# Kernel tuning notes

Hardware: AMD Instinct MI355X
Metric: run time of the kernel (lower is better)

Reference implementation:

```python
import jax, jax.numpy as jnp
import numpy as np

HIDDEN = 4096
NUM_EXPERTS = 64
TOP_K = 2
N_TOKENS = 16384


def setup_inputs() -> dict:
    key = jax.random.key(0)
    kx, kw = jax.random.split(key)
    x = jax.random.normal(kx, (N_TOKENS, HIDDEN), dtype=jnp.float32)
    # nn.Linear(hidden, num_experts, bias=False) weight: [num_experts, hidden]
    gate_w = jax.random.normal(kw, (NUM_EXPERTS, HIDDEN), dtype=jnp.float32) * (HIDDEN ** -0.5)
    return {"x": x, "gate_w": gate_w}


def reference(x, gate_w):
    # logits: [N, num_experts]
    logits = jnp.einsum("nh,eh->ne", x, gate_w)
    topk_vals, topk_idx = jax.lax.top_k(logits, TOP_K)  # [N, k]
    topk_gates = jax.nn.softmax(topk_vals, axis=-1)
    return topk_gates, topk_idx
```

## Files before the change

kernel.cpp:

```cpp
#include <hip/hip_runtime.h>

#define NTOK 16384
#define HID  4096
#define NEXP 64
#define BM   32
#define BK   64
#define NSTEPS (HID / BK)
#define PLANE  (NEXP * HID)

typedef _Float16 f16;
typedef f16  f16x4 __attribute__((ext_vector_type(4)));
typedef f16  f16x8 __attribute__((ext_vector_type(8)));
typedef float f32x4 __attribute__((ext_vector_type(4)));

__device__ __forceinline__ int swz(int row, int unit16) {
    return row * 64 + ((unit16 ^ (row & 7)) << 3);
}

__global__ __launch_bounds__(256)
void pack_w_kernel(const float* __restrict__ w, f16* __restrict__ wp) {
    int tid = blockIdx.x * 256 + threadIdx.x;
    int e = tid >> 9;
    int k = (tid & 511) << 3;
    const float* src = w + (size_t)e * HID + k;
    float4 v0 = *(const float4*)(src);
    float4 v1 = *(const float4*)(src + 4);
    float sv[8] = {v0.x, v0.y, v0.z, v0.w, v1.x, v1.y, v1.z, v1.w};
    f16x8 hi, lo;
    #pragma unroll
    for (int j = 0; j < 8; ++j) {
        float s = sv[j] * 64.0f;
        f16 h = (f16)s;
        hi[j] = h;
        lo[j] = (f16)(s - (float)h);
    }
    int ks   = k >> 5;
    int g    = e >> 4;
    int lane = ((k >> 3) & 3) * 16 + (e & 15);
    size_t dst = ((size_t)(ks * 4 + g) * 64 + lane) * 8;
    *(f16x8*)&wp[dst]         = hi;
    *(f16x8*)&wp[PLANE + dst] = lo;
}

__global__ __launch_bounds__(512, 4)
void topk_gate_kernel(const float* __restrict__ x,
                      const f16* __restrict__ wp,
                      float* __restrict__ out) {
    __shared__ __align__(16) f16 Ah[2][BM * BK];
    __shared__ __align__(16) f16 Al[2][BM * BK];
    __shared__ float red[4][BM][4];

    const int t    = threadIdx.x;
    const int blk  = blockIdx.x;
    const int lane = t & 63;
    const int wid  = t >> 6;
    const int wm   = wid & 1;
    const int wn   = wid >> 1;
    const int col  = lane & 15;
    const int grp  = lane >> 4;

    const int srow = t >> 4;
    const int sq4  = t & 15;
    const float* asrc = x + ((size_t)blk * BM + srow) * HID + sq4 * 4;
    const int aoff = swz(srow, sq4 >> 1) + (sq4 & 1) * 4;

    const f16* bp = wp + ((size_t)(wn * 64 + lane)) * 8;

    f32x4 acc = {0.f, 0.f, 0.f, 0.f};
    const int arow = wm * 16 + col;

    float4 a_cur = *(const float4*)(asrc);
    {
        float4 v = a_cur;
        f16 hx=(f16)v.x, hy=(f16)v.y, hz=(f16)v.z, hw=(f16)v.w;
        *(f16x4*)&Ah[0][aoff] = (f16x4){hx,hy,hz,hw};
        *(f16x4*)&Al[0][aoff] = (f16x4){(f16)(v.x-(float)hx),(f16)(v.y-(float)hy),
                                        (f16)(v.z-(float)hz),(f16)(v.w-(float)hw)};
    }
    float4 a_nxt = *(const float4*)(asrc + BK);
    f16x8 bh0c = *(const f16x8*)(bp + 0);
    f16x8 bl0c = *(const f16x8*)(bp + PLANE + 0);
    f16x8 bh1c = *(const f16x8*)(bp + 2048);
    f16x8 bl1c = *(const f16x8*)(bp + PLANE + 2048);
    __syncthreads();

    for (int s = 0; s < NSTEPS; ++s) {
        const int buf = s & 1;
        const int sn = (s + 1 < NSTEPS) ? (s + 1) : s;
        const size_t bo = (size_t)sn * 4096;
        f16x8 bh0n = *(const f16x8*)(bp + bo);
        f16x8 bl0n = *(const f16x8*)(bp + PLANE + bo);
        f16x8 bh1n = *(const f16x8*)(bp + bo + 2048);
        f16x8 bl1n = *(const f16x8*)(bp + PLANE + bo + 2048);
        float4 a_n2 = (s + 2 < NSTEPS) ? *(const float4*)(asrc + (size_t)(s + 2) * BK)
                                       : a_nxt;

        {
            f16x8 ah = *(const f16x8*)&Ah[buf][swz(arow, grp)];
            f16x8 al = *(const f16x8*)&Al[buf][swz(arow, grp)];
            acc = __builtin_amdgcn_mfma_f32_16x16x32_f16(ah, bh0c, acc, 0, 0, 0);
            acc = __builtin_amdgcn_mfma_f32_16x16x32_f16(ah, bl0c, acc, 0, 0, 0);
            acc = __builtin_amdgcn_mfma_f32_16x16x32_f16(al, bh0c, acc, 0, 0, 0);
            ah = *(const f16x8*)&Ah[buf][swz(arow, 4 + grp)];
            al = *(const f16x8*)&Al[buf][swz(arow, 4 + grp)];
            acc = __builtin_amdgcn_mfma_f32_16x16x32_f16(ah, bh1c, acc, 0, 0, 0);
            acc = __builtin_amdgcn_mfma_f32_16x16x32_f16(ah, bl1c, acc, 0, 0, 0);
            acc = __builtin_amdgcn_mfma_f32_16x16x32_f16(al, bh1c, acc, 0, 0, 0);
        }

        if (s + 1 < NSTEPS) {
            float4 v = a_nxt;
            f16 hx=(f16)v.x, hy=(f16)v.y, hz=(f16)v.z, hw=(f16)v.w;
            *(f16x4*)&Ah[buf ^ 1][aoff] = (f16x4){hx,hy,hz,hw};
            *(f16x4*)&Al[buf ^ 1][aoff] = (f16x4){(f16)(v.x-(float)hx),(f16)(v.y-(float)hy),
                                                  (f16)(v.z-(float)hz),(f16)(v.w-(float)hw)};
        }
        __syncthreads();

        a_nxt = a_n2;
        bh0c = bh0n; bl0c = bl0n; bh1c = bh1n; bl1c = bl1n;
    }

    #pragma unroll
    for (int r = 0; r < 4; ++r) {
        float v0 = acc[r]; int i0 = wn * 16 + col;
        float v1 = -INFINITY; int i1 = 0x7fffffff;
        #pragma unroll
        for (int m = 1; m <= 8; m <<= 1) {
            float ov0 = __shfl_xor(v0, m, 64);
            int   oi0 = __shfl_xor(i0, m, 64);
            float ov1 = __shfl_xor(v1, m, 64);
            int   oi1 = __shfl_xor(i1, m, 64);
            bool ob = (ov0 > v0) || (ov0 == v0 && oi0 < i0);
            if (ob) {
                bool k2 = (v0 > ov1) || (v0 == ov1 && i0 < oi1);
                v1 = k2 ? v0 : ov1; i1 = k2 ? i0 : oi1;
                v0 = ov0; i0 = oi0;
            } else {
                bool k2 = (ov0 > v1) || (ov0 == v1 && oi0 < i1);
                v1 = k2 ? ov0 : v1; i1 = k2 ? oi0 : i1;
            }
        }
        if (col == 0) {
            int tl = wm * 16 + grp * 4 + r;
            red[wn][tl][0] = v0; red[wn][tl][1] = (float)i0;
            red[wn][tl][2] = v1; red[wn][tl][3] = (float)i1;
        }
    }
    __syncthreads();

    if (t < BM) {
        float v0 = red[0][t][0]; int i0 = (int)red[0][t][1];
        float v1 = red[0][t][2]; int i1 = (int)red[0][t][3];
        #pragma unroll
        for (int g = 1; g < 4; ++g) {
            float b0 = red[g][t][0]; int bi0 = (int)red[g][t][1];
            float b1 = red[g][t][2]; int bi1 = (int)red[g][t][3];
            bool bb = (b0 > v0) || (b0 == v0 && bi0 < i0);
            if (bb) {
                bool k2 = (v0 > b1) || (v0 == b1 && i0 < bi1);
                float nv1 = k2 ? v0 : b1; int ni1 = k2 ? i0 : bi1;
                v0 = b0; i0 = bi0; v1 = nv1; i1 = ni1;
            } else {
                bool k2 = (b0 > v1) || (b0 == v1 && bi0 < i1);
                v1 = k2 ? b0 : v1; i1 = k2 ? bi0 : i1;
            }
        }
        float d  = (v1 - v0) * (1.0f / 64.0f);
        float e  = expf(d);
        float g0 = 1.0f / (1.0f + e);
        float g1 = e / (1.0f + e);

        int tok = blk * BM + t;
        out[(size_t)tok * 2 + 0] = g0;
        out[(size_t)tok * 2 + 1] = g1;
        out[(size_t)NTOK * 2 + (size_t)tok * 2 + 0] = (float)i0;
        out[(size_t)NTOK * 2 + (size_t)tok * 2 + 1] = (float)i1;
    }
}

extern "C" void kernel_launch(void* const* d_in, const int* in_sizes, int n_in,
                              void* d_out, int out_size, void* d_ws, size_t ws_size,
                              hipStream_t stream) {
    const float* x = (const float*)d_in[0];
    const float* w = (const float*)d_in[1];
    float* out = (float*)d_out;
    f16* wp = (f16*)d_ws;
    (void)in_sizes; (void)n_in; (void)out_size; (void)ws_size;

    pack_w_kernel<<<dim3(128), dim3(256), 0, stream>>>(w, wp);
    topk_gate_kernel<<<dim3(NTOK / BM), dim3(512), 0, stream>>>(x, wp, out);
}
```

Before: 78.78 us.

## Split K across waves with register-direct A loads and LDS partial-sum reduction

Restructures the gate GEMM so each of four waves covers a quarter of the hidden dimension for all 32 tokens and all 64 experts. A is loaded straight from global memory into registers and split into f16 hi/lo there, which removes the shared-memory staging and the per-step barriers. Partial logits are then summed through LDS, and each wave runs a 64-lane top-2 shuffle reduction per token. This raises per-wave MFMA work and register pressure, and the direct A loads read 32 bytes per row per lane, so coalescing may be worse than before.

New measurement: 73.13 us. 7.2% less time.

```diff
diff --git a/kernel.cpp b/kernel.cpp
--- a/kernel.cpp
+++ b/kernel.cpp
@@ -3,19 +3,15 @@
 #define NTOK 16384
 #define HID  4096
 #define NEXP 64
-#define BM   32
-#define BK   64
-#define NSTEPS (HID / BK)
+#define TOKB 32
+#define KSPLIT 4
+#define STEPS (HID / KSPLIT / 64)
 #define PLANE  (NEXP * HID)
+#define LROW 68
 
 typedef _Float16 f16;
-typedef f16  f16x4 __attribute__((ext_vector_type(4)));
 typedef f16  f16x8 __attribute__((ext_vector_type(8)));
 typedef float f32x4 __attribute__((ext_vector_type(4)));
-
-__device__ __forceinline__ int swz(int row, int unit16) {
-    return row * 64 + ((unit16 ^ (row & 7)) << 3);
-}
 
 __global__ __launch_bounds__(256)
 void pack_w_kernel(const float* __restrict__ w, f16* __restrict__ wp) {
@@ -42,91 +38,129 @@
     *(f16x8*)&wp[PLANE + dst] = lo;
 }
 
-__global__ __launch_bounds__(512, 4)
+__device__ __forceinline__ void cvt_hilo(float4 a, float4 b, f16x8& hi, f16x8& lo) {
+    float v[8] = {a.x, a.y, a.z, a.w, b.x, b.y, b.z, b.w};
+    #pragma unroll
+    for (int j = 0; j < 8; ++j) {
+        f16 h = (f16)v[j];
+        hi[j] = h;
+        lo[j] = (f16)(v[j] - (float)h);
+    }
+}
+
+__global__ __launch_bounds__(256)
 void topk_gate_kernel(const float* __restrict__ x,
                       const f16* __restrict__ wp,
                       float* __restrict__ out) {
-    __shared__ __align__(16) f16 Ah[2][BM * BK];
-    __shared__ __align__(16) f16 Al[2][BM * BK];
-    __shared__ float red[4][BM][4];
+    __shared__ float P[KSPLIT][TOKB * LROW];
+    __shared__ float F[TOKB * LROW];
 
     const int t    = threadIdx.x;
     const int blk  = blockIdx.x;
     const int lane = t & 63;
-    const int wid  = t >> 6;
-    const int wm   = wid & 1;
-    const int wn   = wid >> 1;
+    const int w    = t >> 6;
     const int col  = lane & 15;
     const int grp  = lane >> 4;
 
-    const int srow = t >> 4;
-    const int sq4  = t & 15;
-    const float* asrc = x + ((size_t)blk * BM + srow) * HID + sq4 * 4;
-    const int aoff = swz(srow, sq4 >> 1) + (sq4 & 1) * 4;
-
-    const f16* bp = wp + ((size_t)(wn * 64 + lane)) * 8;
-
-    f32x4 acc = {0.f, 0.f, 0.f, 0.f};
-    const int arow = wm * 16 + col;
-
-    float4 a_cur = *(const float4*)(asrc);
+    const float* aw = x + ((size_t)blk * TOKB + col) * HID + w * (HID / KSPLIT) + grp * 8;
+    const f16* bw = wp + (size_t)lane * 8;
+
+    f32x4 acc[2][4];
+    #pragma unroll
+    for (int tm = 0; tm < 2; ++tm)
+        #pragma unroll
+        for (int eg = 0; eg < 4; ++eg)
+            acc[tm][eg] = (f32x4){0.f, 0.f, 0.f, 0.f};
+
+    float4 af[2][2][2];
+    #pragma unroll
+    for (int tm = 0; tm < 2; ++tm)
+        #pragma unroll
+        for (int ks = 0; ks < 2; ++ks)
+            #pragma unroll
+            for (int h = 0; h < 2; ++h)
+                af[tm][ks][h] = *(const float4*)(aw + tm * 16 * HID + ks * 32 + h * 4);
+
+    for (int s = 0; s < STEPS; ++s) {
+        f16x8 bh[2][4], bl[2][4];
+        #pragma unroll
+        for (int ks = 0; ks < 2; ++ks) {
+            const size_t base = (size_t)((w * 32 + s * 2 + ks) * 4) * 512;
+            #pragma unroll
+            for (int eg = 0; eg < 4; ++eg) {
+                bh[ks][eg] = *(const f16x8*)(bw + base + eg * 512);
+                bl[ks][eg] = *(const f16x8*)(bw + base + eg * 512 + PLANE);
+            }
+        }
+        const int sn = (s + 1 < STEPS) ? (s + 1) : s;
+        float4 an[2][2][2];
+        #pragma unroll
+        for (int tm = 0; tm < 2; ++tm)
+            #pragma unroll
+            for (int ks = 0; ks < 2; ++ks)
+                #pragma unroll
+                for (int h = 0; h < 2; ++h)
+                    an[tm][ks][h] = *(const float4*)(aw + tm * 16 * HID + sn * 64 + ks * 32 + h * 4);
+
+        f16x8 ah[2][2], al[2][2];
+        #pragma unroll
+        for (int tm = 0; tm < 2; ++tm)
+            #pragma unroll
+            for (int ks = 0; ks < 2; ++ks)
+                cvt_hilo(af[tm][ks][0], af[tm][ks][1], ah[tm][ks], al[tm][ks]);
+
+        #pragma unroll
+        for (int ks = 0; ks < 2; ++ks)
+            #pragma unroll
+            for (int tm = 0; tm < 2; ++tm)
+                #pragma unroll
+                for (int eg = 0; eg < 4; ++eg) {
+                    acc[tm][eg] = __builtin_amdgcn_mfma_f32_16x16x32_f16(ah[tm][ks], bh[ks][eg], acc[tm][eg], 0, 0, 0);
+                    acc[tm][eg] = __builtin_amdgcn_mfma_f32_16x16x32_f16(ah[tm][ks], bl[ks][eg], acc[tm][eg], 0, 0, 0);
+                    acc[tm][eg] = __builtin_amdgcn_mfma_f32_16x16x32_f16(al[tm][ks], bh[ks][eg], acc[tm][eg], 0, 0, 0);
+                }
+
+        #pragma unroll
+        for (int tm = 0; tm < 2; ++tm)
+            #pragma unroll
+            for (int ks = 0; ks < 2; ++ks)
+                #pragma unroll
+                for (int h = 0; h < 2; ++h)
+                    af[tm][ks][h] = an[tm][ks][h];
+    }
+
+    #pragma unroll
+    for (int tm = 0; tm < 2; ++tm)
+        #pragma unroll
+        for (int eg = 0; eg < 4; ++eg)
+            #pragma unroll
+            for (int r = 0; r < 4; ++r) {
+                int tokl = tm * 16 + grp * 4 + r;
+                int e    = eg * 16 + col;
+                P[w][tokl * LROW + e] = acc[tm][eg][r];
+            }
+    __syncthreads();
+
     {
-        float4 v = a_cur;
-        f16 hx=(f16)v.x, hy=(f16)v.y, hz=(f16)v.z, hw=(f16)v.w;
-        *(f16x4*)&Ah[0][aoff] = (f16x4){hx,hy,hz,hw};
-        *(f16x4*)&Al[0][aoff] = (f16x4){(f16)(v.x-(float)hx),(f16)(v.y-(float)hy),
-                                        (f16)(v.z-(float)hz),(f16)(v.w-(float)hw)};
-    }
-    float4 a_nxt = *(const float4*)(asrc + BK);
-    f16x8 bh0c = *(const f16x8*)(bp + 0);
-    f16x8 bl0c = *(const f16x8*)(bp + PLANE + 0);
-    f16x8 bh1c = *(const f16x8*)(bp + 2048);
-    f16x8 bl1c = *(const f16x8*)(bp + PLANE + 2048);
+        int tok = t >> 3;
+        int e0  = (t & 7) * 8;
+        #pragma unroll
+        for (int j = 0; j < 8; ++j) {
+            float ssum = P[0][tok * LROW + e0 + j];
+            #pragma unroll
+            for (int w2 = 1; w2 < KSPLIT; ++w2)
+                ssum += P[w2][tok * LROW + e0 + j];
+            F[tok * LROW + e0 + j] = ssum;
+        }
+    }
     __syncthreads();
 
-    for (int s = 0; s < NSTEPS; ++s) {
-        const int buf = s & 1;
-        const int sn = (s + 1 < NSTEPS) ? (s + 1) : s;
-        const size_t bo = (size_t)sn * 4096;
-        f16x8 bh0n = *(const f16x8*)(bp + bo);
-        f16x8 bl0n = *(const f16x8*)(bp + PLANE + bo);
-        f16x8 bh1n = *(const f16x8*)(bp + bo + 2048);
-        f16x8 bl1n = *(const f16x8*)(bp + PLANE + bo + 2048);
-        float4 a_n2 = (s + 2 < NSTEPS) ? *(const float4*)(asrc + (size_t)(s + 2) * BK)
-                                       : a_nxt;
-
-        {
-            f16x8 ah = *(const f16x8*)&Ah[buf][swz(arow, grp)];
-            f16x8 al = *(const f16x8*)&Al[buf][swz(arow, grp)];
-            acc = __builtin_amdgcn_mfma_f32_16x16x32_f16(ah, bh0c, acc, 0, 0, 0);
-            acc = __builtin_amdgcn_mfma_f32_16x16x32_f16(ah, bl0c, acc, 0, 0, 0);
-            acc = __builtin_amdgcn_mfma_f32_16x16x32_f16(al, bh0c, acc, 0, 0, 0);
-            ah = *(const f16x8*)&Ah[buf][swz(arow, 4 + grp)];
-            al = *(const f16x8*)&Al[buf][swz(arow, 4 + grp)];
-            acc = __builtin_amdgcn_mfma_f32_16x16x32_f16(ah, bh1c, acc, 0, 0, 0);
-            acc = __builtin_amdgcn_mfma_f32_16x16x32_f16(ah, bl1c, acc, 0, 0, 0);
-            acc = __builtin_amdgcn_mfma_f32_16x16x32_f16(al, bh1c, acc, 0, 0, 0);
-        }
-
-        if (s + 1 < NSTEPS) {
-            float4 v = a_nxt;
-            f16 hx=(f16)v.x, hy=(f16)v.y, hz=(f16)v.z, hw=(f16)v.w;
-            *(f16x4*)&Ah[buf ^ 1][aoff] = (f16x4){hx,hy,hz,hw};
-            *(f16x4*)&Al[buf ^ 1][aoff] = (f16x4){(f16)(v.x-(float)hx),(f16)(v.y-(float)hy),
-                                                  (f16)(v.z-(float)hz),(f16)(v.w-(float)hw)};
-        }
-        __syncthreads();
-
-        a_nxt = a_n2;
-        bh0c = bh0n; bl0c = bl0n; bh1c = bh1n; bl1c = bl1n;
-    }
-
-    #pragma unroll
-    for (int r = 0; r < 4; ++r) {
-        float v0 = acc[r]; int i0 = wn * 16 + col;
-        float v1 = -INFINITY; int i1 = 0x7fffffff;
-        #pragma unroll
-        for (int m = 1; m <= 8; m <<= 1) {
+    for (int tt = 0; tt < 8; ++tt) {
+        int tokl = w * 8 + tt;
+        float v0 = F[tokl * LROW + lane]; int i0 = lane;
+        float v1 = -INFINITY;             int i1 = 0x7fffffff;
+        #pragma unroll
+        for (int m = 1; m <= 32; m <<= 1) {
             float ov0 = __shfl_xor(v0, m, 64);
             int   oi0 = __shfl_xor(i0, m, 64);
             float ov1 = __shfl_xor(v1, m, 64);
@@ -141,41 +175,17 @@
                 v1 = k2 ? ov0 : v1; i1 = k2 ? oi0 : i1;
             }
         }
-        if (col == 0) {
-            int tl = wm * 16 + grp * 4 + r;
-            red[wn][tl][0] = v0; red[wn][tl][1] = (float)i0;
-            red[wn][tl][2] = v1; red[wn][tl][3] = (float)i1;
-        }
-    }
-    __syncthreads();
-
-    if (t < BM) {
-        float v0 = red[0][t][0]; int i0 = (int)red[0][t][1];
-        float v1 = red[0][t][2]; int i1 = (int)red[0][t][3];
-        #pragma unroll
-        for (int g = 1; g < 4; ++g) {
-            float b0 = red[g][t][0]; int bi0 = (int)red[g][t][1];
-            float b1 = red[g][t][2]; int bi1 = (int)red[g][t][3];
-            bool bb = (b0 > v0) || (b0 == v0 && bi0 < i0);
-            if (bb) {
-                bool k2 = (v0 > b1) || (v0 == b1 && i0 < bi1);
-                float nv1 = k2 ? v0 : b1; int ni1 = k2 ? i0 : bi1;
-                v0 = b0; i0 = bi0; v1 = nv1; i1 = ni1;
-            } else {
-                bool k2 = (b0 > v1) || (b0 == v1 && bi0 < i1);
-                v1 = k2 ? b0 : v1; i1 = k2 ? bi0 : i1;
-            }
-        }
-        float d  = (v1 - v0) * (1.0f / 64.0f);
-        float e  = expf(d);
-        float g0 = 1.0f / (1.0f + e);
-        float g1 = e / (1.0f + e);
-
-        int tok = blk * BM + t;
-        out[(size_t)tok * 2 + 0] = g0;
-        out[(size_t)tok * 2 + 1] = g1;
-        out[(size_t)NTOK * 2 + (size_t)tok * 2 + 0] = (float)i0;
-        out[(size_t)NTOK * 2 + (size_t)tok * 2 + 1] = (float)i1;
+        if (lane == 0) {
+            float d  = (v1 - v0) * (1.0f / 64.0f);
+            float e  = expf(d);
+            float g0 = 1.0f / (1.0f + e);
+            float g1 = e / (1.0f + e);
+            int tok = blk * TOKB + tokl;
+            out[(size_t)tok * 2 + 0] = g0;
+            out[(size_t)tok * 2 + 1] = g1;
+            out[(size_t)NTOK * 2 + (size_t)tok * 2 + 0] = (float)i0;
+            out[(size_t)NTOK * 2 + (size_t)tok * 2 + 1] = (float)i1;
+        }
     }
 }
 
@@ -189,5 +199,5 @@
     (void)in_sizes; (void)n_in; (void)out_size; (void)ws_size;
 
     pack_w_kernel<<<dim3(128), dim3(256), 0, stream>>>(w, wp);
-    topk_gate_kernel<<<dim3(NTOK / BM), dim3(512), 0, stream>>>(x, wp, out);
-}
+    topk_gate_kernel<<<dim3(NTOK / TOKB), dim3(256), 0, stream>>>(x, wp, out);
+}
```

## Stream activations via direct global-to-LDS loads with triple-buffered pipeline

Applied to the files above, without the earlier changes.

Replaces the register-staged fp32 load and split-to-fp16 store with global_load_lds DMA straight into a three-deep LDS ring of raw fp32 activations. The hi/lo fp16 split now happens after reading from LDS, right before the MFMAs. Weight fragments are prefetched two steps ahead, and a manual vmcnt wait plus one barrier per step replaces the old end-of-step sync. This is meant to hide global latency and cut VGPR staging traffic, but it doubles the LDS footprint per buffer and relies on a hand-tuned vmcnt count being correct.

Measured after the change: 96.64 us. 22.7% more time.

```diff
diff --git a/kernel.cpp b/kernel.cpp
--- a/kernel.cpp
+++ b/kernel.cpp
@@ -1,21 +1,19 @@
 #include <hip/hip_runtime.h>
+#include <stdint.h>
 
 #define NTOK 16384
 #define HID  4096
 #define NEXP 64
-#define BM   32
-#define BK   64
-#define NSTEPS (HID / BK)
-#define PLANE  (NEXP * HID)
+#define TOKB 32
+#define NSTEPS 64
+#define PLANE (NEXP * HID)
 
 typedef _Float16 f16;
-typedef f16  f16x4 __attribute__((ext_vector_type(4)));
 typedef f16  f16x8 __attribute__((ext_vector_type(8)));
 typedef float f32x4 __attribute__((ext_vector_type(4)));
 
-__device__ __forceinline__ int swz(int row, int unit16) {
-    return row * 64 + ((unit16 ^ (row & 7)) << 3);
-}
+typedef __attribute__((address_space(3))) uint32_t  lds_u32;
+typedef __attribute__((address_space(1))) const uint32_t glb_u32;
 
 __global__ __launch_bounds__(256)
 void pack_w_kernel(const float* __restrict__ w, f16* __restrict__ wp) {
@@ -46,84 +44,100 @@
 void topk_gate_kernel(const float* __restrict__ x,
                       const f16* __restrict__ wp,
                       float* __restrict__ out) {
-    __shared__ __align__(16) f16 Ah[2][BM * BK];
-    __shared__ __align__(16) f16 Al[2][BM * BK];
-    __shared__ float red[4][BM][4];
+    __shared__ __align__(16) float Abuf[3][TOKB * 64];
+    __shared__ float red[4][TOKB][4];
 
     const int t    = threadIdx.x;
     const int blk  = blockIdx.x;
     const int lane = t & 63;
-    const int wid  = t >> 6;
-    const int wm   = wid & 1;
-    const int wn   = wid >> 1;
+    const int w    = t >> 6;
+    const int tm   = w & 1;
+    const int eg   = w >> 1;
     const int col  = lane & 15;
     const int grp  = lane >> 4;
 
-    const int srow = t >> 4;
-    const int sq4  = t & 15;
-    const float* asrc = x + ((size_t)blk * BM + srow) * HID + sq4 * 4;
-    const int aoff = swz(srow, sq4 >> 1) + (sq4 & 1) * 4;
-
-    const f16* bp = wp + ((size_t)(wn * 64 + lane)) * 8;
+    const int srow  = 4 * w + grp;
+    const int sunit = col ^ (srow & 7);
+    const float* asrc = x + ((size_t)blk * TOKB + srow) * HID + sunit * 4;
+
+    int fragOff[2][2];
+    {
+        const int arow = tm * 16 + col;
+        #pragma unroll
+        for (int ks = 0; ks < 2; ++ks)
+            #pragma unroll
+            for (int h = 0; h < 2; ++h)
+                fragOff[ks][h] = arow * 256 + ((ks * 8 + grp * 2 + h) ^ (arow & 7)) * 16;
+    }
+
+    const f16* bw = wp + ((size_t)eg * 64 + lane) * 8;
 
     f32x4 acc = {0.f, 0.f, 0.f, 0.f};
-    const int arow = wm * 16 + col;
-
-    float4 a_cur = *(const float4*)(asrc);
-    {
-        float4 v = a_cur;
-        f16 hx=(f16)v.x, hy=(f16)v.y, hz=(f16)v.z, hw=(f16)v.w;
-        *(f16x4*)&Ah[0][aoff] = (f16x4){hx,hy,hz,hw};
-        *(f16x4*)&Al[0][aoff] = (f16x4){(f16)(v.x-(float)hx),(f16)(v.y-(float)hy),
-                                        (f16)(v.z-(float)hz),(f16)(v.w-(float)hw)};
-    }
-    float4 a_nxt = *(const float4*)(asrc + BK);
-    f16x8 bh0c = *(const f16x8*)(bp + 0);
-    f16x8 bl0c = *(const f16x8*)(bp + PLANE + 0);
-    f16x8 bh1c = *(const f16x8*)(bp + 2048);
-    f16x8 bl1c = *(const f16x8*)(bp + PLANE + 2048);
-    __syncthreads();
-
+
+    #define STAGE(s_, b_) do {                                                    \
+        __builtin_amdgcn_global_load_lds(                                         \
+            (glb_u32*)(const void*)(asrc + (size_t)(s_) * 64),                    \
+            (lds_u32*)(void*)(&Abuf[b_][w * 256]), 16, 0, 0);                     \
+    } while (0)
+
+    f16x8 bh0[2], bl0[2], bh1[2], bl1[2], bh2[2], bl2[2];
+    #define BLOAD(s_, BH, BL) do {                                                \
+        _Pragma("unroll")                                                         \
+        for (int ks = 0; ks < 2; ++ks) {                                          \
+            size_t off_ = (size_t)(2 * (s_) + ks) * 2048;                         \
+            BH[ks] = *(const f16x8*)(bw + off_);                                  \
+            BL[ks] = *(const f16x8*)(bw + off_ + PLANE);                          \
+        }                                                                         \
+    } while (0)
+
+    STAGE(0, 0);
+    BLOAD(0, bh0, bl0);
+    asm volatile("" ::: "memory");
+    BLOAD(1, bh1, bl1);
+    asm volatile("" ::: "memory");
+    STAGE(1, 1);
+
+    int bufc = 0;
     for (int s = 0; s < NSTEPS; ++s) {
-        const int buf = s & 1;
-        const int sn = (s + 1 < NSTEPS) ? (s + 1) : s;
-        const size_t bo = (size_t)sn * 4096;
-        f16x8 bh0n = *(const f16x8*)(bp + bo);
-        f16x8 bl0n = *(const f16x8*)(bp + PLANE + bo);
-        f16x8 bh1n = *(const f16x8*)(bp + bo + 2048);
-        f16x8 bl1n = *(const f16x8*)(bp + PLANE + bo + 2048);
-        float4 a_n2 = (s + 2 < NSTEPS) ? *(const float4*)(asrc + (size_t)(s + 2) * BK)
-                                       : a_nxt;
-
-        {
-            f16x8 ah = *(const f16x8*)&Ah[buf][swz(arow, grp)];
-            f16x8 al = *(const f16x8*)&Al[buf][swz(arow, grp)];
-            acc = __builtin_amdgcn_mfma_f32_16x16x32_f16(ah, bh0c, acc, 0, 0, 0);
-            acc = __builtin_amdgcn_mfma_f32_16x16x32_f16(ah, bl0c, acc, 0, 0, 0);
-            acc = __builtin_amdgcn_mfma_f32_16x16x32_f16(al, bh0c, acc, 0, 0, 0);
-            ah = *(const f16x8*)&Ah[buf][swz(arow, 4 + grp)];
-            al = *(const f16x8*)&Al[buf][swz(arow, 4 + grp)];
-            acc = __builtin_amdgcn_mfma_f32_16x16x32_f16(ah, bh1c, acc, 0, 0, 0);
-            acc = __builtin_amdgcn_mfma_f32_16x16x32_f16(ah, bl1c, acc, 0, 0, 0);
-            acc = __builtin_amdgcn_mfma_f32_16x16x32_f16(al, bh1c, acc, 0, 0, 0);
-        }
-
-        if (s + 1 < NSTEPS) {
-            float4 v = a_nxt;
-            f16 hx=(f16)v.x, hy=(f16)v.y, hz=(f16)v.z, hw=(f16)v.w;
-            *(f16x4*)&Ah[buf ^ 1][aoff] = (f16x4){hx,hy,hz,hw};
-            *(f16x4*)&Al[buf ^ 1][aoff] = (f16x4){(f16)(v.x-(float)hx),(f16)(v.y-(float)hy),
-                                                  (f16)(v.z-(float)hz),(f16)(v.w-(float)hw)};
-        }
-        __syncthreads();
-
-        a_nxt = a_n2;
-        bh0c = bh0n; bl0c = bl0n; bh1c = bh1n; bl1c = bl1n;
+        asm volatile("s_waitcnt vmcnt(5)" ::: "memory");
+        __builtin_amdgcn_s_barrier();
+        asm volatile("" ::: "memory");
+
+        const int s2 = (s + 2 < NSTEPS) ? s + 2 : NSTEPS - 1;
+        BLOAD(s2, bh2, bl2);
+        asm volatile("" ::: "memory");
+        int bufn = bufc + 2; if (bufn >= 3) bufn -= 3;
+        STAGE(s2, bufn);
+
+        const char* bp = (const char*)&Abuf[bufc][0];
+        #pragma unroll
+        for (int ks = 0; ks < 2; ++ks) {
+            float4 q0 = *(const float4*)(bp + fragOff[ks][0]);
+            float4 q1 = *(const float4*)(bp + fragOff[ks][1]);
+            float v[8] = {q0.x, q0.y, q0.z, q0.w, q1.x, q1.y, q1.z, q1.w};
+            f16x8 ah, al;
+            #pragma unroll
+            for (int j = 0; j < 8; ++j) {
+                f16 h = (f16)v[j];
+                ah[j] = h;
+                al[j] = (f16)(v[j] - (float)h);
+            }
+            acc = __builtin_amdgcn_mfma_f32_16x16x32_f16(ah, bh0[ks], acc, 0, 0, 0);
+            acc = __builtin_amdgcn_mfma_f32_16x16x32_f16(ah, bl0[ks], acc, 0, 0, 0);
+            acc = __builtin_amdgcn_mfma_f32_16x16x32_f16(al, bh0[ks], acc, 0, 0, 0);
+        }
+
+        #pragma unroll
+        for (int ks = 0; ks < 2; ++ks) {
+            bh0[ks] = bh1[ks]; bl0[ks] = bl1[ks];
+            bh1[ks] = bh2[ks]; bl1[ks] = bl2[ks];
+        }
+        if (++bufc == 3) bufc = 0;
     }
 
     #pragma unroll
     for (int r = 0; r < 4; ++r) {
-        float v0 = acc[r]; int i0 = wn * 16 + col;
+        float v0 = acc[r]; int i0 = eg * 16 + col;
         float v1 = -INFINITY; int i1 = 0x7fffffff;
         #pragma unroll
         for (int m = 1; m <= 8; m <<= 1) {
@@ -142,14 +156,14 @@
             }
         }
         if (col == 0) {
-            int tl = wm * 16 + grp * 4 + r;
-            red[wn][tl][0] = v0; red[wn][tl][1] = (float)i0;
-            red[wn][tl][2] = v1; red[wn][tl][3] = (float)i1;
+            int tl = tm * 16 + grp * 4 + r;
+            red[eg][tl][0] = v0; red[eg][tl][1] = (float)i0;
+            red[eg][tl][2] = v1; red[eg][tl][3] = (float)i1;
         }
     }
     __syncthreads();
 
-    if (t < BM) {
+    if (t < TOKB) {
         float v0 = red[0][t][0]; int i0 = (int)red[0][t][1];
         float v1 = red[0][t][2]; int i1 = (int)red[0][t][3];
         #pragma unroll
@@ -171,7 +185,7 @@
         float g0 = 1.0f / (1.0f + e);
         float g1 = e / (1.0f + e);
 
-        int tok = blk * BM + t;
+        int tok = blk * TOKB + t;
         out[(size_t)tok * 2 + 0] = g0;
         out[(size_t)tok * 2 + 1] = g1;
         out[(size_t)NTOK * 2 + (size_t)tok * 2 + 0] = (float)i0;
@@ -189,5 +203,5 @@
     (void)in_sizes; (void)n_in; (void)out_size; (void)ws_size;
 
     pack_w_kernel<<<dim3(128), dim3(256), 0, stream>>>(w, wp);
-    topk_gate_kernel<<<dim3(NTOK / BM), dim3(512), 0, stream>>>(x, wp, out);
+    topk_gate_kernel<<<dim3(NTOK / TOKB), dim3(512), 0, stream>>>(x, wp, out);
 }
```
